# Optimization experiments

Measured on AMD Instinct MI355X. Metric: run time of the kernel, lower is better.

Reference implementation:

```python
import jax, jax.numpy as jnp
import numpy as np


def silu(x):
    return x * jax.nn.sigmoid(x)


def conv1x1(x, w, s, b, act):
    # x: [B,Ci,H,W], w: [Co,Ci]; BN folded into per-channel scale s / bias b
    y = jnp.einsum('oi,bihw->bohw', w, x) * s[None, :, None, None] + b[None, :, None, None]
    return silu(y) if act else y


def dwconv3x3(x, w, s, b):
    # depthwise 3x3, groups=C, padding SAME (autopad=1); w: [C,1,3,3]
    y = jax.lax.conv_general_dilated(
        x, w, window_strides=(1, 1), padding=[(1, 1), (1, 1)],
        dimension_numbers=('NCHW', 'OIHW', 'NCHW'),
        feature_group_count=x.shape[1])
    return y * s[None, :, None, None] + b[None, :, None, None]


def attention(x, qkv_w, qkv_s, qkv_b, pe_w, pe_s, pe_b, proj_w, proj_s, proj_b,
              num_heads=4, key_dim=32, head_dim=64):
    B, C, H, W = x.shape
    N = H * W
    scale = key_dim ** -0.5
    qkv = conv1x1(x, qkv_w, qkv_s, qkv_b, act=False)          # [B, C+2*nh*kd, H, W]
    qkv = qkv.reshape(B, num_heads, key_dim * 2 + head_dim, N)
    q = qkv[:, :, :key_dim]                                    # [B,nh,kd,N]
    k = qkv[:, :, key_dim:2 * key_dim]                         # [B,nh,kd,N]
    v = qkv[:, :, 2 * key_dim:]                                # [B,nh,hd,N]
    attn = jnp.einsum('bhdi,bhdj->bhij', q, k) * scale         # [B,nh,N,N]
    attn = jax.nn.softmax(attn, axis=-1)
    out = jnp.einsum('bhdj,bhij->bhdi', v, attn)               # [B,nh,hd,N]
    out = out.reshape(B, C, H, W) + dwconv3x3(v.reshape(B, C, H, W), pe_w, pe_s, pe_b)
    return conv1x1(out, proj_w, proj_s, proj_b, act=False)


def setup_inputs() -> dict:
    key = jax.random.key(0)
    ks = jax.random.split(key, 32)
    B, C1, H, W = 4, 512, 48, 48
    c = C1 // 2  # 256
    h = c + 2 * 32 * 4  # 512
    d = {'x': jax.random.normal(ks[0], (B, C1, H, W), jnp.float32)}
    def w(i, shape):
        return jax.random.normal(ks[i], shape, jnp.float32) * 0.05
    def s(i, n):
        return jax.random.uniform(ks[i], (n,), jnp.float32, 0.5, 1.5)
    def b(i, n):
        return jax.random.normal(ks[i], (n,), jnp.float32) * 0.05
    d['cv1_w'], d['cv1_s'], d['cv1_b'] = w(1, (2 * c, C1)), s(2, 2 * c), b(3, 2 * c)
    d['qkv_w'], d['qkv_s'], d['qkv_b'] = w(4, (h, c)), s(5, h), b(6, h)
    d['pe_w'], d['pe_s'], d['pe_b'] = w(7, (c, 1, 3, 3)), s(8, c), b(9, c)
    d['proj_w'], d['proj_s'], d['proj_b'] = w(10, (c, c)), s(11, c), b(12, c)
    d['ffn1_w'], d['ffn1_s'], d['ffn1_b'] = w(13, (2 * c, c)), s(14, 2 * c), b(15, 2 * c)
    d['ffn2_w'], d['ffn2_s'], d['ffn2_b'] = w(16, (c, 2 * c)), s(17, c), b(18, c)
    d['cv2_w'], d['cv2_s'], d['cv2_b'] = w(19, (C1, 2 * c)), s(20, C1), b(21, C1)
    return d


def reference(x, cv1_w, cv1_s, cv1_b, qkv_w, qkv_s, qkv_b, pe_w, pe_s, pe_b,
              proj_w, proj_s, proj_b, ffn1_w, ffn1_s, ffn1_b, ffn2_w, ffn2_s, ffn2_b,
              cv2_w, cv2_s, cv2_b):
    c = cv1_w.shape[0] // 2  # hidden channels (256)
    ab = conv1x1(x, cv1_w, cv1_s, cv1_b, act=True)
    a, bb = ab[:, :c], ab[:, c:]
    bb = bb + attention(bb, qkv_w, qkv_s, qkv_b, pe_w, pe_s, pe_b,
                        proj_w, proj_s, proj_b)
    f = conv1x1(bb, ffn1_w, ffn1_s, ffn1_b, act=True)
    bb = bb + conv1x1(f, ffn2_w, ffn2_s, ffn2_b, act=False)
    return conv1x1(jnp.concatenate([a, bb], axis=1), cv2_w, cv2_s, cv2_b, act=True)
```

## Files before the change

### kernel.cpp

```cpp
#include <hip/hip_runtime.h>
#include <math.h>

#define N_SP 2304
#define HW 48

typedef unsigned short u16;
typedef short s8v  __attribute__((ext_vector_type(8)));
typedef short s4v  __attribute__((ext_vector_type(4)));
typedef u16   u16x8 __attribute__((ext_vector_type(8)));
typedef float f32x4 __attribute__((ext_vector_type(4)));
typedef unsigned u32x4 __attribute__((ext_vector_type(4)));

__device__ __forceinline__ short f2bf(float x) {
    unsigned u = __float_as_uint(x);
    u += 0x7FFFu + ((u >> 16) & 1u);
    return (short)(u >> 16);
}
__device__ __forceinline__ float bf2f(u16 u) {
    return __uint_as_float((unsigned)u << 16);
}
__device__ __forceinline__ float fexp2(float x) { return __builtin_amdgcn_exp2f(x); }
__device__ __forceinline__ float frcp(float x)  { return __builtin_amdgcn_rcpf(x); }
__device__ __forceinline__ float fsilu(float v) {
    return v * frcp(1.f + fexp2(-1.4426950408889634f * v));
}
__device__ __forceinline__ unsigned cvtpk(float lo, float hi) {
    unsigned r;
    asm("v_cvt_pk_bf16_f32 %0, %1, %2" : "=v"(r) : "v"(lo), "v"(hi));
    return r;
}
__device__ __forceinline__ void gload16(const void* g, void* l) {
    __builtin_amdgcn_global_load_lds(
        (const __attribute__((address_space(1))) void*)g,
        (__attribute__((address_space(3))) void*)l, 16, 0, 0);
}
__device__ __forceinline__ void bar_lgkm() {
    asm volatile("s_waitcnt lgkmcnt(0)" ::: "memory");
    __builtin_amdgcn_s_barrier();
}

__global__ __launch_bounds__(256) void prep(
    const float* __restrict__ X, u16* __restrict__ XT,
    const float* __restrict__ s0, const float* __restrict__ s1,
    const float* __restrict__ s2, const float* __restrict__ s3,
    const float* __restrict__ s4, const float* __restrict__ s5,
    u16* __restrict__ d0, u16* __restrict__ d1, u16* __restrict__ d2,
    u16* __restrict__ d3, u16* __restrict__ d4, u16* __restrict__ d5)
{
    __shared__ float tile[64][65];
    const int t = threadIdx.x;
    if (blockIdx.x < 960) {
        int id = blockIdx.x * 256 + t;
        const int c0 = 65536, c1 = c0 + 32768, c2 = c1 + 16384,
                  c3 = c2 + 32768, c4 = c3 + 32768, c5 = c4 + 65536;
        if (id >= c5) return;
        const float* s; u16* d; int off;
        if      (id < c0) { s = s0; d = d0; off = id; }
        else if (id < c1) { s = s1; d = d1; off = id - c0; }
        else if (id < c2) { s = s2; d = d2; off = id - c1; }
        else if (id < c3) { s = s3; d = d3; off = id - c2; }
        else if (id < c4) { s = s4; d = d4; off = id - c3; }
        else              { s = s5; d = d5; off = id - c4; }
        float4 v = ((const float4*)s)[off];
        s4v p; p[0] = f2bf(v.x); p[1] = f2bf(v.y); p[2] = f2bf(v.z); p[3] = f2bf(v.w);
        ((s4v*)d)[off] = p;
        return;
    }
    const int bid = blockIdx.x - 960;
    const int n0 = (bid % 36) * 64, c0 = ((bid / 36) & 7) * 64, b = bid / 288;
    const float* src = X + (long)b * 512 * N_SP;
    u16* dst = XT + (long)b * N_SP * 512;
    #pragma unroll
    for (int it = 0; it < 16; ++it) {
        int id = t + 256 * it;
        int cl = id >> 6, nl = id & 63;
        tile[cl][nl] = src[(long)(c0 + cl) * N_SP + n0 + nl];
    }
    __syncthreads();
    #pragma unroll
    for (int it = 0; it < 16; ++it) {
        int id = t + 256 * it;
        int nl = id >> 6, cl = id & 63;
        dst[(long)(n0 + nl) * 512 + c0 + cl] = f2bf(tile[cl][nl]);
    }
}

template <int NO, int OMODE>
__global__ __launch_bounds__(256) void mfma_gemm(
    const u16* __restrict__ A1, const u16* __restrict__ A2, int K1,
    int sA1, int sA2, int K,
    const u16* __restrict__ W,
    const float* __restrict__ S, const float* __restrict__ Bi,
    const u16* __restrict__ Res, int sR,
    void* __restrict__ OutP, int sO, int Mtot,
    int act)
{
    __shared__ u16 Al[3][64][64];
    __shared__ u16 Bl[3][64][64];
    const int t  = threadIdx.x;
    const int p = blockIdx.x;
    const int cx = p & 7, q = p >> 3;
    const int n0 = (cx * 18 + q / NO) * 64;
    const int o0 = (q % NO) * 64;
    const int lane = t & 63, w = t >> 6;
    const int wn = (w & 1) * 32, wo = (w >> 1) * 32;
    const int li = lane & 15, g = lane >> 4;

    const int b_blk = n0 / N_SP;
    const int n_in0 = n0 - b_blk * N_SP;

    f32x4 acc[2][2];
    #pragma unroll
    for (int fm = 0; fm < 2; ++fm)
        #pragma unroll
        for (int fn = 0; fn < 2; ++fn) acc[fm][fn] = f32x4{0.f, 0.f, 0.f, 0.f};

    auto issue = [&](int buf, int k0) {
        #pragma unroll
        for (int qq = 0; qq < 2; ++qq) {
            int c = t + qq * 256;
            int row = c >> 3;
            int col = ((c & 7) ^ (row & 7)) * 8;
            int kk = k0 + col;
            const u16* ga = (kk < K1) ? (A1 + (long)(n0 + row) * sA1 + kk)
                                      : (A2 + (long)(n0 + row) * sA2 + (kk - K1));
            gload16(ga, (u16*)Al[buf] + (qq * 256 + w * 64) * 8);
            gload16(W + (long)(o0 + row) * K + k0 + col,
                    (u16*)Bl[buf] + (qq * 256 + w * 64) * 8);
        }
    };

    const int NK = K >> 6;
    issue(0, 0);
    if (NK > 1) issue(1, 64);

    for (int ks = 0; ks < NK; ++ks) {
        if (ks + 1 < NK) asm volatile("s_waitcnt vmcnt(4)" ::: "memory");
        else             asm volatile("s_waitcnt vmcnt(0)" ::: "memory");
        __builtin_amdgcn_s_barrier();
        if (ks + 2 < NK) issue((ks + 2) % 3, (ks + 2) << 6);
        const int cur = ks % 3;
        #pragma unroll
        for (int k2 = 0; k2 < 2; ++k2) {
            s8v af[2], bfv[2];
            #pragma unroll
            for (int fm = 0; fm < 2; ++fm) {
                int row = wn + fm * 16 + li;
                af[fm] = *(const s8v*)&Al[cur][row][((g + 4 * k2) ^ (li & 7)) * 8];
            }
            #pragma unroll
            for (int fn = 0; fn < 2; ++fn) {
                int row = wo + fn * 16 + li;
                bfv[fn] = *(const s8v*)&Bl[cur][row][((g + 4 * k2) ^ (li & 7)) * 8];
            }
            #pragma unroll
            for (int fm = 0; fm < 2; ++fm)
                #pragma unroll
                for (int fn = 0; fn < 2; ++fn)
                    acc[fm][fn] = __builtin_amdgcn_mfma_f32_16x16x32_bf16(
                        af[fm], bfv[fn], acc[fm][fn], 0, 0, 0);
        }
    }

    #pragma unroll
    for (int fn = 0; fn < 2; ++fn) {
        const int o = o0 + wo + fn * 16 + li;
        const float sc2 = S[o], bi = Bi[o];
        #pragma unroll
        for (int fm = 0; fm < 2; ++fm) {
            const int nb  = n0 + wn + fm * 16 + 4 * g;
            const int nib = n_in0 + wn + fm * 16 + 4 * g;
            float y[4];
            #pragma unroll
            for (int r = 0; r < 4; ++r) {
                float v = acc[fm][fn][r] * sc2 + bi;
                if (act) v = fsilu(v);
                y[r] = v;
            }
            if (Res) {
                #pragma unroll
                for (int r = 0; r < 4; ++r)
                    y[r] += bf2f(Res[(long)(nb + r) * sR + o]);
            }
            if (OMODE == 0) {
                u16* O = (u16*)OutP;
                #pragma unroll
                for (int r = 0; r < 4; ++r)
                    O[(long)(nb + r) * sO + o] = (u16)f2bf(y[r]);
            } else if (OMODE == 1) {
                u16* O = (u16*)OutP + (long)b_blk * Mtot * N_SP + (long)o * N_SP + nib;
                s4v pk;
                #pragma unroll
                for (int r = 0; r < 4; ++r) pk[r] = f2bf(y[r]);
                *(s4v*)O = pk;
            } else {
                float* O = (float*)OutP + (long)b_blk * Mtot * N_SP + (long)o * N_SP + nib;
                *(float4*)O = make_float4(y[0], y[1], y[2], y[3]);
            }
        }
    }
}

__global__ __launch_bounds__(256) void attn_mfma(const u16* __restrict__ qkv,
    u16* __restrict__ Opart, float* __restrict__ mpart, float* __restrict__ lpart)
{
    const int N = N_SP;
    __shared__ u16 Klds[2][64][40];
    __shared__ u16 Vlds[2][64][72];

    const int p = blockIdx.x;
    const int cx = p & 7, q = p >> 3;
    const int i0 = (q % 18) * 128;
    const int bhz = cx + 8 * (q / 18);
    const int bh = bhz & 15, z = bhz >> 4;
    const int b = bh >> 2, h = bh & 3;
    const int t = threadIdx.x;
    const int w = t >> 6;
    const int lane = t & 63;
    const int li = lane & 15;
    const int g  = lane >> 4;
    const float qscale = 0.17677669529663687f * 1.4426950408889634f;

    const u16* qp = qkv + ((long)b * 512 + (long)h * 128) * N;
    const u16* kp = qp + 32L * N;
    const u16* vp = qp + 64L * N;

    const int ia = i0 + w * 16 + li;
    const int ib = ia + 64;

    s8v qf[2];
    #pragma unroll
    for (int r = 0; r < 8; ++r) {
        qf[0][r] = f2bf(bf2f(qp[(long)(8 * g + r) * N + ia]) * qscale);
        qf[1][r] = f2bf(bf2f(qp[(long)(8 * g + r) * N + ib]) * qscale);
    }

    f32x4 oacc[2][4];
    #pragma unroll
    for (int q2 = 0; q2 < 2; ++q2)
        #pragma unroll
        for (int dt = 0; dt < 4; ++dt) oacc[q2][dt] = f32x4{0.f, 0.f, 0.f, 0.f};
    float m_run[2] = {-1e30f, -1e30f}, l_run[2] = {0.f, 0.f};

    const int kj  = lane;
    const int kd0 = w * 8;
    const int vd  = t >> 2;
    const int vjb = (t & 3) * 16;

    const int jbase = z * 576;
    u16x8 kr, vr0, vr1;
    auto ldregs = [&](int j0) {
        const u16* kpp = kp + j0 + kj;
        #pragma unroll
        for (int u = 0; u < 8; ++u) kr[u] = kpp[(long)(kd0 + u) * N];
        vr0 = *(const u16x8*)(vp + (long)vd * N + j0 + vjb);
        vr1 = *(const u16x8*)(vp + (long)vd * N + j0 + vjb + 8);
    };

    ldregs(jbase);
    *(u16x8*)&Klds[0][kj][kd0]     = kr;
    *(u16x8*)&Vlds[0][vd][vjb]     = vr0;
    *(u16x8*)&Vlds[0][vd][vjb + 8] = vr1;
    ldregs(jbase + 64);
    bar_lgkm();

    int cur = 0;
    for (int it = 0; it < 9; ++it) {
        if (it + 1 < 9) {
            *(u16x8*)&Klds[cur ^ 1][kj][kd0]     = kr;
            *(u16x8*)&Vlds[cur ^ 1][vd][vjb]     = vr0;
            *(u16x8*)&Vlds[cur ^ 1][vd][vjb + 8] = vr1;
            if (it + 2 < 9) ldregs(jbase + (it + 2) * 64);
        }

        f32x4 sacc[2][4];
        #pragma unroll
        for (int js = 0; js < 4; ++js) {
            s8v kf = *(const s8v*)&Klds[cur][js * 16 + li][8 * g];
            f32x4 zz = f32x4{0.f, 0.f, 0.f, 0.f};
            sacc[0][js] = __builtin_amdgcn_mfma_f32_16x16x32_bf16(kf, qf[0], zz, 0, 0, 0);
            sacc[1][js] = __builtin_amdgcn_mfma_f32_16x16x32_bf16(kf, qf[1], zz, 0, 0, 0);
        }

        #pragma unroll
        for (int q2 = 0; q2 < 2; ++q2) {
            float tm = -1e30f;
            #pragma unroll
            for (int js = 0; js < 4; ++js)
                #pragma unroll
                for (int r = 0; r < 4; ++r) tm = fmaxf(tm, sacc[q2][js][r]);
            tm = fmaxf(tm, __shfl_xor(tm, 16, 64));
            tm = fmaxf(tm, __shfl_xor(tm, 32, 64));
            if (__any(tm > m_run[q2] + 8.f)) {
                float mnew = fmaxf(m_run[q2], tm);
                float scl  = fexp2(m_run[q2] - mnew);
                l_run[q2] *= scl;
                #pragma unroll
                for (int dt = 0; dt < 4; ++dt) oacc[q2][dt] *= scl;
                m_run[q2] = mnew;
            }
            float ts = 0.f;
            #pragma unroll
            for (int js = 0; js < 4; ++js)
                #pragma unroll
                for (int r = 0; r < 4; ++r) {
                    float pv = fexp2(sacc[q2][js][r] - m_run[q2]);
                    sacc[q2][js][r] = pv;
                    ts += pv;
                }
            ts += __shfl_xor(ts, 16, 64);
            ts += __shfl_xor(ts, 32, 64);
            l_run[q2] += ts;
        }

        #pragma unroll
        for (int ks = 0; ks < 2; ++ks) {
            s8v pf[2];
            #pragma unroll
            for (int q2 = 0; q2 < 2; ++q2) {
                u32x4 pw;
                pw[0] = cvtpk(sacc[q2][2 * ks][0],     sacc[q2][2 * ks][1]);
                pw[1] = cvtpk(sacc[q2][2 * ks][2],     sacc[q2][2 * ks][3]);
                pw[2] = cvtpk(sacc[q2][2 * ks + 1][0], sacc[q2][2 * ks + 1][1]);
                pw[3] = cvtpk(sacc[q2][2 * ks + 1][2], sacc[q2][2 * ks + 1][3]);
                pf[q2] = __builtin_bit_cast(s8v, pw);
            }
            #pragma unroll
            for (int dt = 0; dt < 4; ++dt) {
                int d = dt * 16 + li;
                s4v lo = *(const s4v*)&Vlds[cur][d][32 * ks + 4 * g];
                s4v hi = *(const s4v*)&Vlds[cur][d][32 * ks + 16 + 4 * g];
                s8v vf = __builtin_shufflevector(lo, hi, 0, 1, 2, 3, 4, 5, 6, 7);
                oacc[0][dt] = __builtin_amdgcn_mfma_f32_16x16x32_bf16(vf, pf[0], oacc[0][dt], 0, 0, 0);
                oacc[1][dt] = __builtin_amdgcn_mfma_f32_16x16x32_bf16(vf, pf[1], oacc[1][dt], 0, 0, 0);
            }
        }

        if (it + 1 < 9) bar_lgkm();
        cur ^= 1;
    }

    const long cb = (long)(z * 16 + bh);
    #pragma unroll
    for (int q2 = 0; q2 < 2; ++q2) {
        const int i = q2 ? ib : ia;
        #pragma unroll
        for (int dt = 0; dt < 4; ++dt)
            #pragma unroll
            for (int r = 0; r < 4; ++r)
                Opart[(cb * 64 + dt * 16 + 4 * g + r) * N + i] = (u16)f2bf(oacc[q2][dt][r]);
        if (g == 0) {
            mpart[cb * N + i] = m_run[q2];
            lpart[cb * N + i] = l_run[q2];
        }
    }
}

__global__ __launch_bounds__(256) void attn_combine(
    const u16* __restrict__ Opart, const float* __restrict__ mpart,
    const float* __restrict__ lpart, const u16* __restrict__ qkv,
    const float* __restrict__ pw, const float* __restrict__ ps,
    const float* __restrict__ pb, u16* __restrict__ attnT)
{
    const int N = N_SP;
    const int i0 = blockIdx.x * 64;
    const int bh = blockIdx.y;
    const int b = bh >> 2, h = bh & 3;
    const int t = threadIdx.x;
    const int il = t & 63, dq = t >> 6;
    const int d0 = dq * 16;
    const int i = i0 + il;

    float mm[4], ll[4];
    #pragma unroll
    for (int c = 0; c < 4; ++c) {
        mm[c] = mpart[((long)(c * 16 + bh)) * N + i];
        ll[c] = lpart[((long)(c * 16 + bh)) * N + i];
    }
    float ms = fmaxf(fmaxf(mm[0], mm[1]), fmaxf(mm[2], mm[3]));
    float wc[4], lsum = 0.f;
    #pragma unroll
    for (int c = 0; c < 4; ++c) {
        wc[c] = fexp2(mm[c] - ms);
        lsum += wc[c] * ll[c];
    }
    float inv = frcp(lsum);

    const int y = i / HW, x = i - (i / HW) * HW;
    const int y0ok = (y > 0), y1ok = (y < HW - 1);
    const int x0ok = (x > 0), x1ok = (x < HW - 1);
    const u16* vbase = qkv + ((long)b * 512 + (long)h * 128 + 64) * N;

    u16 ob[16];
    #pragma unroll
    for (int dd = 0; dd < 16; ++dd) {
        const int d = d0 + dd;
        const int cg = h * 64 + d;
        float o = 0.f;
        #pragma unroll
        for (int c = 0; c < 4; ++c)
            o += wc[c] * bf2f(Opart[((long)(c * 16 + bh) * 64 + d) * N + i]);
        o *= inv;
        const u16* src = vbase + (long)d * N;
        const float* w9 = pw + cg * 9;
        float s = 0.f;
        #pragma unroll
        for (int dy = -1; dy <= 1; ++dy) {
            if ((dy < 0 && !y0ok) || (dy > 0 && !y1ok)) continue;
            const u16* row = src + (y + dy) * HW;
            if (x0ok) s += w9[(dy + 1) * 3 + 0] * bf2f(row[x - 1]);
            s += w9[(dy + 1) * 3 + 1] * bf2f(row[x]);
            if (x1ok) s += w9[(dy + 1) * 3 + 2] * bf2f(row[x + 1]);
        }
        o += s * ps[cg] + pb[cg];
        ob[dd] = (u16)f2bf(o);
    }
    u16* dst = attnT + ((long)b * N + i) * 256 + h * 64 + d0;
    *(u16x8*)dst       = *(u16x8*)&ob[0];
    *(u16x8*)(dst + 8) = *(u16x8*)&ob[8];
}

extern "C" void kernel_launch(void* const* d_in, const int* in_sizes, int n_in,
                              void* d_out, int out_size, void* d_ws, size_t ws_size,
                              hipStream_t stream)
{
    const long N = N_SP;
    const float* x      = (const float*)d_in[0];
    const float* cv1_w  = (const float*)d_in[1];
    const float* cv1_s  = (const float*)d_in[2];
    const float* cv1_b  = (const float*)d_in[3];
    const float* qkv_w  = (const float*)d_in[4];
    const float* qkv_s  = (const float*)d_in[5];
    const float* qkv_b  = (const float*)d_in[6];
    const float* pe_w   = (const float*)d_in[7];
    const float* pe_s   = (const float*)d_in[8];
    const float* pe_b   = (const float*)d_in[9];
    const float* proj_w = (const float*)d_in[10];
    const float* proj_s = (const float*)d_in[11];
    const float* proj_b = (const float*)d_in[12];
    const float* ffn1_w = (const float*)d_in[13];
    const float* ffn1_s = (const float*)d_in[14];
    const float* ffn1_b = (const float*)d_in[15];
    const float* ffn2_w = (const float*)d_in[16];
    const float* ffn2_s = (const float*)d_in[17];
    const float* ffn2_b = (const float*)d_in[18];
    const float* cv2_w  = (const float*)d_in[19];
    const float* cv2_s  = (const float*)d_in[20];
    const float* cv2_b  = (const float*)d_in[21];
    float* out = (float*)d_out;

    u16* ws = (u16*)d_ws;
    u16* xT      = ws;
    u16* abT     = xT      + 4L * N * 512;
    u16* qkvb    = abT     + 4L * N * 512;
    u16* attnT   = qkvb    + 4L * N * 512;
    u16* bb2T    = attnT   + 4L * N * 256;
    u16* fT      = bb2T    + 4L * N * 256;
    u16* bb3T    = fT      + 4L * N * 512;
    u16* w_cv1   = bb3T    + 4L * N * 256;
    u16* w_qkv   = w_cv1   + 512L * 512;
    u16* w_proj  = w_qkv   + 512L * 256;
    u16* w_ffn1  = w_proj  + 256L * 256;
    u16* w_ffn2  = w_ffn1  + 512L * 256;
    u16* w_cv2   = w_ffn2  + 256L * 512;
    u16* Opart   = w_cv2   + 512L * 512;
    float* mpart = (float*)(Opart + 4L * 16 * 64 * N);
    float* lpart = mpart + 4L * 16 * N;

    dim3 blk(256);
    const int BIGK = 1 << 28;

    prep<<<2112, blk, 0, stream>>>(x, xT,
        cv1_w, qkv_w, proj_w, ffn1_w, ffn2_w, cv2_w,
        w_cv1, w_qkv, w_proj, w_ffn1, w_ffn2, w_cv2);

    mfma_gemm<8, 0><<<1152, blk, 0, stream>>>(
        xT, nullptr, BIGK, 512, 0, 512, w_cv1, cv1_s, cv1_b,
        nullptr, 0, abT, 512, 512, 1);

    mfma_gemm<8, 1><<<1152, blk, 0, stream>>>(
        abT + 256, nullptr, BIGK, 512, 0, 256, w_qkv, qkv_s, qkv_b,
        nullptr, 0, qkvb, 0, 512, 0);

    attn_mfma<<<1152, blk, 0, stream>>>(qkvb, Opart, mpart, lpart);

    attn_combine<<<dim3(36, 16), blk, 0, stream>>>(
        Opart, mpart, lpart, qkvb, pe_w, pe_s, pe_b, attnT);

    mfma_gemm<4, 0><<<576, blk, 0, stream>>>(
        attnT, nullptr, BIGK, 256, 0, 256, w_proj, proj_s, proj_b,
        abT + 256, 512, bb2T, 256, 256, 0);

    mfma_gemm<8, 0><<<1152, blk, 0, stream>>>(
        bb2T, nullptr, BIGK, 256, 0, 256, w_ffn1, ffn1_s, ffn1_b,
        nullptr, 0, fT, 512, 512, 1);

    mfma_gemm<4, 0><<<576, blk, 0, stream>>>(
        fT, nullptr, BIGK, 512, 0, 512, w_ffn2, ffn2_s, ffn2_b,
        bb2T, 256, bb3T, 256, 256, 0);

    mfma_gemm<8, 2><<<1152, blk, 0, stream>>>(
        abT, bb3T, 256, 512, 256, 512, w_cv2, cv2_s, cv2_b,
        nullptr, 0, out, 0, 512, 1);
}
```

Baseline: 145.5 us.

## Emit token-major QKV copy for vectorized Q/K loads; raise MFMA wave priority

The QKV GEMM now also writes a transposed token-major bf16 copy, so the attention kernel can load Q and K rows as 16-byte vectors instead of eight strided scalar loads each. MFMA sections in the attention loop are wrapped with s_setprio to favor matrix issue. This adds an extra scattered 2-byte-per-element store pass in the GEMM epilogue and extra workspace traffic in exchange for cheaper attention loads.

```diff
diff --git a/kernel.cpp b/kernel.cpp
--- a/kernel.cpp
+++ b/kernel.cpp
@@ -92,7 +92,7 @@
     const u16* __restrict__ W,
     const float* __restrict__ S, const float* __restrict__ Bi,
     const u16* __restrict__ Res, int sR,
-    void* __restrict__ OutP, int sO, int Mtot,
+    void* __restrict__ OutP, u16* __restrict__ OutT, int sO, int Mtot,
     int act)
 {
     __shared__ u16 Al[3][64][64];
@@ -187,12 +187,17 @@
                 #pragma unroll
                 for (int r = 0; r < 4; ++r)
                     O[(long)(nb + r) * sO + o] = (u16)f2bf(y[r]);
-            } else if (OMODE == 1) {
+            } else if (OMODE == 1 || OMODE == 3) {
                 u16* O = (u16*)OutP + (long)b_blk * Mtot * N_SP + (long)o * N_SP + nib;
                 s4v pk;
                 #pragma unroll
                 for (int r = 0; r < 4; ++r) pk[r] = f2bf(y[r]);
                 *(s4v*)O = pk;
+                if (OMODE == 3) {
+                    #pragma unroll
+                    for (int r = 0; r < 4; ++r)
+                        OutT[(long)(nb + r) * 512 + o] = (u16)f2bf(y[r]);
+                }
             } else {
                 float* O = (float*)OutP + (long)b_blk * Mtot * N_SP + (long)o * N_SP + nib;
                 *(float4*)O = make_float4(y[0], y[1], y[2], y[3]);
@@ -202,6 +207,7 @@
 }
 
 __global__ __launch_bounds__(256) void attn_mfma(const u16* __restrict__ qkv,
+    const u16* __restrict__ qkvT,
     u16* __restrict__ Opart, float* __restrict__ mpart, float* __restrict__ lpart)
 {
     const int N = N_SP;
@@ -221,18 +227,22 @@
     const int g  = lane >> 4;
     const float qscale = 0.17677669529663687f * 1.4426950408889634f;
 
-    const u16* qp = qkv + ((long)b * 512 + (long)h * 128) * N;
-    const u16* kp = qp + 32L * N;
-    const u16* vp = qp + 64L * N;
+    const u16* qp  = qkv  + ((long)b * 512 + (long)h * 128) * N;
+    const u16* vp  = qp + 64L * N;
+    const u16* qTp = qkvT + (long)b * N * 512 + h * 128;
 
     const int ia = i0 + w * 16 + li;
     const int ib = ia + 64;
 
     s8v qf[2];
-    #pragma unroll
-    for (int r = 0; r < 8; ++r) {
-        qf[0][r] = f2bf(bf2f(qp[(long)(8 * g + r) * N + ia]) * qscale);
-        qf[1][r] = f2bf(bf2f(qp[(long)(8 * g + r) * N + ib]) * qscale);
+    {
+        s8v qa = *(const s8v*)(qTp + (long)ia * 512 + 8 * g);
+        s8v qb = *(const s8v*)(qTp + (long)ib * 512 + 8 * g);
+        #pragma unroll
+        for (int r = 0; r < 8; ++r) {
+            qf[0][r] = f2bf(bf2f((u16)qa[r]) * qscale);
+            qf[1][r] = f2bf(bf2f((u16)qb[r]) * qscale);
+        }
     }
 
     f32x4 oacc[2][4];
@@ -242,23 +252,21 @@
         for (int dt = 0; dt < 4; ++dt) oacc[q2][dt] = f32x4{0.f, 0.f, 0.f, 0.f};
     float m_run[2] = {-1e30f, -1e30f}, l_run[2] = {0.f, 0.f};
 
-    const int kj  = lane;
-    const int kd0 = w * 8;
+    const int kj2 = t & 63;
+    const int kd  = (t >> 6) * 8;
     const int vd  = t >> 2;
     const int vjb = (t & 3) * 16;
 
     const int jbase = z * 576;
     u16x8 kr, vr0, vr1;
     auto ldregs = [&](int j0) {
-        const u16* kpp = kp + j0 + kj;
-        #pragma unroll
-        for (int u = 0; u < 8; ++u) kr[u] = kpp[(long)(kd0 + u) * N];
+        kr  = *(const u16x8*)(qTp + (long)(j0 + kj2) * 512 + 32 + kd);
         vr0 = *(const u16x8*)(vp + (long)vd * N + j0 + vjb);
         vr1 = *(const u16x8*)(vp + (long)vd * N + j0 + vjb + 8);
     };
 
     ldregs(jbase);
-    *(u16x8*)&Klds[0][kj][kd0]     = kr;
+    *(u16x8*)&Klds[0][kj2][kd]     = kr;
     *(u16x8*)&Vlds[0][vd][vjb]     = vr0;
     *(u16x8*)&Vlds[0][vd][vjb + 8] = vr1;
     ldregs(jbase + 64);
@@ -267,13 +275,14 @@
     int cur = 0;
     for (int it = 0; it < 9; ++it) {
         if (it + 1 < 9) {
-            *(u16x8*)&Klds[cur ^ 1][kj][kd0]     = kr;
+            *(u16x8*)&Klds[cur ^ 1][kj2][kd]     = kr;
             *(u16x8*)&Vlds[cur ^ 1][vd][vjb]     = vr0;
             *(u16x8*)&Vlds[cur ^ 1][vd][vjb + 8] = vr1;
             if (it + 2 < 9) ldregs(jbase + (it + 2) * 64);
         }
 
         f32x4 sacc[2][4];
+        __builtin_amdgcn_s_setprio(1);
         #pragma unroll
         for (int js = 0; js < 4; ++js) {
             s8v kf = *(const s8v*)&Klds[cur][js * 16 + li][8 * g];
@@ -281,6 +290,7 @@
             sacc[0][js] = __builtin_amdgcn_mfma_f32_16x16x32_bf16(kf, qf[0], zz, 0, 0, 0);
             sacc[1][js] = __builtin_amdgcn_mfma_f32_16x16x32_bf16(kf, qf[1], zz, 0, 0, 0);
         }
+        __builtin_amdgcn_s_setprio(0);
 
         #pragma unroll
         for (int q2 = 0; q2 < 2; ++q2) {
@@ -313,6 +323,7 @@
             l_run[q2] += ts;
         }
 
+        __builtin_amdgcn_s_setprio(1);
         #pragma unroll
         for (int ks = 0; ks < 2; ++ks) {
             s8v pf[2];
@@ -335,6 +346,7 @@
                 oacc[1][dt] = __builtin_amdgcn_mfma_f32_16x16x32_bf16(vf, pf[1], oacc[1][dt], 0, 0, 0);
             }
         }
+        __builtin_amdgcn_s_setprio(0);
 
         if (it + 1 < 9) bar_lgkm();
         cur ^= 1;
@@ -453,7 +465,8 @@
     u16* xT      = ws;
     u16* abT     = xT      + 4L * N * 512;
     u16* qkvb    = abT     + 4L * N * 512;
-    u16* attnT   = qkvb    + 4L * N * 512;
+    u16* qkvT    = qkvb    + 4L * N * 512;
+    u16* attnT   = qkvT    + 4L * N * 512;
     u16* bb2T    = attnT   + 4L * N * 256;
     u16* fT      = bb2T    + 4L * N * 256;
     u16* bb3T    = fT      + 4L * N * 512;
@@ -476,30 +489,30 @@
 
     mfma_gemm<8, 0><<<1152, blk, 0, stream>>>(
         xT, nullptr, BIGK, 512, 0, 512, w_cv1, cv1_s, cv1_b,
-        nullptr, 0, abT, 512, 512, 1);
-
-    mfma_gemm<8, 1><<<1152, blk, 0, stream>>>(
+        nullptr, 0, abT, nullptr, 512, 512, 1);
+
+    mfma_gemm<8, 3><<<1152, blk, 0, stream>>>(
         abT + 256, nullptr, BIGK, 512, 0, 256, w_qkv, qkv_s, qkv_b,
-        nullptr, 0, qkvb, 0, 512, 0);
-
-    attn_mfma<<<1152, blk, 0, stream>>>(qkvb, Opart, mpart, lpart);
+        nullptr, 0, qkvb, qkvT, 0, 512, 0);
+
+    attn_mfma<<<1152, blk, 0, stream>>>(qkvb, qkvT, Opart, mpart, lpart);
 
     attn_combine<<<dim3(36, 16), blk, 0, stream>>>(
         Opart, mpart, lpart, qkvb, pe_w, pe_s, pe_b, attnT);
 
     mfma_gemm<4, 0><<<576, blk, 0, stream>>>(
         attnT, nullptr, BIGK, 256, 0, 256, w_proj, proj_s, proj_b,
-        abT + 256, 512, bb2T, 256, 256, 0);
+        abT + 256, 512, bb2T, nullptr, 256, 256, 0);
 
     mfma_gemm<8, 0><<<1152, blk, 0, stream>>>(
         bb2T, nullptr, BIGK, 256, 0, 256, w_ffn1, ffn1_s, ffn1_b,
-        nullptr, 0, fT, 512, 512, 1);
+        nullptr, 0, fT, nullptr, 512, 512, 1);
 
     mfma_gemm<4, 0><<<576, blk, 0, stream>>>(
         fT, nullptr, BIGK, 512, 0, 512, w_ffn2, ffn2_s, ffn2_b,
-        bb2T, 256, bb3T, 256, 256, 0);
+        bb2T, 256, bb3T, nullptr, 256, 256, 0);
 
     mfma_gemm<8, 2><<<1152, blk, 0, stream>>>(
         abT, bb3T, 256, 512, 256, 512, w_cv2, cv2_s, cv2_b,
-        nullptr, 0, out, 0, 512, 1);
-}
+        nullptr, 0, out, nullptr, 0, 512, 1);
+}
```

Result: no change. 146.5 us (+0.7%).
